# Optimization experiments

Measured on AMD Instinct MI355X. Metric: run time of the kernel, lower is better.

Reference implementation:

```python
import jax, jax.numpy as jnp
import numpy as np

B, S_IMG, S_TXT = 1, 3072, 512
D_MODEL, H, D_HEAD = 3072, 24, 128
INNER = H * D_HEAD
EPS = 1e-5


def rms_norm(x, w):
    # x: [..., D_HEAD]
    var = jnp.mean(jnp.square(x), axis=-1, keepdims=True)
    return x * jax.lax.rsqrt(var + EPS) * w


def apply_rope(x, cos, sin):
    # x: [B,S,H,D]; cos/sin: [S,D]; interleaved (non-neox) rotation
    x1 = x[..., 0::2]
    x2 = x[..., 1::2]
    rot = jnp.stack([-x2, x1], axis=-1).reshape(x.shape)
    c = cos[None, :, None, :]
    s = sin[None, :, None, :]
    return x * c + rot * s


def setup_inputs() -> dict:
    key = jax.random.key(0)
    ks = jax.random.split(key, 12)
    sc = 1.0 / np.sqrt(D_MODEL)
    ang = jax.random.uniform(ks[10], (S_TXT + S_IMG, D_HEAD), jnp.float32, 0.0, 2 * np.pi)
    return {
        "hidden_states": jax.random.normal(ks[0], (B, S_IMG, D_MODEL), jnp.float32),
        "encoder_hidden_states": jax.random.normal(ks[1], (B, S_TXT, D_MODEL), jnp.float32),
        "cos": jnp.cos(ang),
        "sin": jnp.sin(ang),
        "W_qkv": jax.random.normal(ks[2], (3 * INNER, D_MODEL), jnp.float32) * sc,
        "W_add_qkv": jax.random.normal(ks[3], (3 * INNER, D_MODEL), jnp.float32) * sc,
        "b_add_qkv": jnp.zeros((3 * INNER,), jnp.float32),
        "norm_q_w": jnp.ones((D_HEAD,), jnp.float32),
        "norm_k_w": jnp.ones((D_HEAD,), jnp.float32),
        "norm_add_q_w": jnp.ones((D_HEAD,), jnp.float32),
        "norm_add_k_w": jnp.ones((D_HEAD,), jnp.float32),
        "W_out": jax.random.normal(ks[4], (D_MODEL, INNER), jnp.float32) * sc,
        "b_out": jnp.zeros((D_MODEL,), jnp.float32),
        "W_add_out": jax.random.normal(ks[5], (D_MODEL, INNER), jnp.float32) * sc,
        "b_add_out": jnp.zeros((D_MODEL,), jnp.float32),
    }


def reference(hidden_states, encoder_hidden_states, cos, sin,
              W_qkv, W_add_qkv, b_add_qkv,
              norm_q_w, norm_k_w, norm_add_q_w, norm_add_k_w,
              W_out, b_out, W_add_out, b_add_out):
    # fused QKV projections
    qkv = jnp.einsum('bsd,ed->bse', hidden_states, W_qkv)
    q, k, v = jnp.split(qkv, 3, axis=-1)
    eqkv = jnp.einsum('bsd,ed->bse', encoder_hidden_states, W_add_qkv) + b_add_qkv
    eq, ek, ev = jnp.split(eqkv, 3, axis=-1)

    def heads(x):
        return x.reshape(x.shape[0], x.shape[1], H, D_HEAD)

    q, k, v = heads(q), heads(k), heads(v)
    eq, ek, ev = heads(eq), heads(ek), heads(ev)

    # per-head RMSNorm on queries/keys
    q = rms_norm(q, norm_q_w)
    k = rms_norm(k, norm_k_w)
    eq = rms_norm(eq, norm_add_q_w)
    ek = rms_norm(ek, norm_add_k_w)

    # joint concat: text first, then image
    q = jnp.concatenate([eq, q], axis=1)
    k = jnp.concatenate([ek, k], axis=1)
    v = jnp.concatenate([ev, v], axis=1)

    # RoPE on full joint sequence
    q = apply_rope(q, cos, sin)
    k = apply_rope(k, cos, sin)

    # non-causal softmax attention, scale = 1/sqrt(head_dim)
    scale = 1.0 / np.sqrt(D_HEAD)
    scores = jnp.einsum('bqhd,bkhd->bhqk', q, k) * scale
    probs = jax.nn.softmax(scores, axis=-1)
    out = jnp.einsum('bhqk,bkhd->bqhd', probs, v)  # [B,S,H,D]
    out = out.reshape(out.shape[0], out.shape[1], INNER)

    enc_out = out[:, :S_TXT]
    img_out = out[:, S_TXT:]
    enc_out = jnp.einsum('bse,de->bsd', enc_out, W_add_out) + b_add_out
    img_out = jnp.einsum('bse,de->bsd', img_out, W_out) + b_out
    return (img_out, enc_out)
```

## Files before the change

### kernel.cpp

```cpp
#include <hip/hip_runtime.h>


typedef unsigned short u16;
typedef __attribute__((ext_vector_type(2))) unsigned short u16x2;
typedef __attribute__((ext_vector_type(4))) unsigned short u16x4;
typedef __attribute__((ext_vector_type(8))) unsigned short u16x8;
typedef __attribute__((ext_vector_type(8))) short bf16x8;
typedef __attribute__((ext_vector_type(4))) float f32x4;

#define DEV __device__ __forceinline__

DEV u16 f2bf(float f) {
  unsigned u = __builtin_bit_cast(unsigned, f);
  u = (u + 0x7FFFu + ((u >> 16) & 1u)) >> 16;
  return (u16)u;
}
DEV float bf2f(u16 s) { return __builtin_bit_cast(float, (unsigned)s << 16); }

DEV void store_out(u16* p, float v)  { *p = f2bf(v); }
DEV void store_out(float* p, float v) { *p = v; }

#define AS1(p) (const __attribute__((address_space(1))) void*)(p)
#define AS3(p) (__attribute__((address_space(3))) void*)(p)
#define GLL16(g, l) __builtin_amdgcn_global_load_lds(AS1(g), AS3(l), 16, 0, 0)

#define BAR() do { asm volatile("" ::: "memory"); __builtin_amdgcn_s_barrier(); \
                   asm volatile("" ::: "memory"); } while (0)
#define VMC8() asm volatile("s_waitcnt vmcnt(8)" ::: "memory")
#define VMC0() asm volatile("s_waitcnt vmcnt(0)" ::: "memory")

__global__ __launch_bounds__(256) void cvt_kernel(const float* __restrict__ src,
                                                  u16* __restrict__ dst, int n4) {
  int i = blockIdx.x * blockDim.x + threadIdx.x;
  int stride = gridDim.x * blockDim.x;
  for (; i < n4; i += stride) {
    float4 v = reinterpret_cast<const float4*>(src)[i];
    u16x4 o;
    o.x = f2bf(v.x); o.y = f2bf(v.y); o.z = f2bf(v.z); o.w = f2bf(v.w);
    reinterpret_cast<u16x4*>(dst)[i] = o;
  }
}

template <typename OT>
__global__ __launch_bounds__(512, 2) void gemm256(
    const u16* __restrict__ A,
    const u16* __restrict__ Bimg, const u16* __restrict__ Benc,
    const float* __restrict__ biasImg, const float* __restrict__ biasEnc,
    OT* __restrict__ Cimg, OT* __restrict__ Cenc,
    int N, int K, int split, int nwg) {
  const int bid = blockIdx.x;
  const int swz = (bid & 7) * (nwg >> 3) + (bid >> 3);
  const int ntn = N >> 8;
  const int mt = swz / ntn, nt = swz % ntn;
  const int m0 = mt << 8, n0 = nt << 8;
  const u16* B = (m0 < split) ? Benc : Bimg;
  const float* bias = (m0 < split) ? biasEnc : biasImg;

  __shared__ u16 lds[2][2][16384];

  const int tid = threadIdx.x, w = tid >> 6, lane = tid & 63;
  const int wm = w >> 2, wn = w & 3;
  const int q = lane & 15, hi = lane >> 4;
  const size_t ldb = (size_t)K * 2;

  f32x4 acc[8][4];
#pragma unroll
  for (int i = 0; i < 8; ++i)
#pragma unroll
    for (int j = 0; j < 4; ++j)
#pragma unroll
      for (int r = 0; r < 4; ++r) acc[i][j][r] = 0.f;

  auto STAGE = [&](int d, int kt) {
    const char* sA = (const char*)A + (size_t)m0 * ldb + kt * 128;
    const char* sB = (const char*)B + (size_t)n0 * ldb + kt * 128;
    char* dA = (char*)&lds[d][0][0];
    char* dB = (char*)&lds[d][1][0];
#pragma unroll
    for (int j = 0; j < 4; ++j) {
      int base = j * 8192 + w * 1024;
      int off = base + lane * 16;
      int row = off >> 7;
      int src = (off & 127) ^ ((row & 7) << 4);
      GLL16(sA + (size_t)row * ldb + src, dA + base);
      GLL16(sB + (size_t)row * ldb + src, dB + base);
    }
  };
  auto LDA = [&](int d, int i, int ks) -> bf16x8 {
    int row = wm * 128 + i * 16 + q;
    int cb = ks * 64 + hi * 16;
    return *(const bf16x8*)((const char*)&lds[d][0][0] + row * 128 + (cb ^ ((row & 7) << 4)));
  };
  auto LDB = [&](int d, int j, int ks) -> bf16x8 {
    int row = wn * 64 + j * 16 + q;
    int cb = ks * 64 + hi * 16;
    return *(const bf16x8*)((const char*)&lds[d][1][0] + row * 128 + (cb ^ ((row & 7) << 4)));
  };

  auto HALF = [&](int d) {
    bf16x8 bfr[4][2];
#pragma unroll
    for (int ph = 0; ph < 4; ++ph) {
      if (ph == 0) {
#pragma unroll
        for (int j = 0; j < 4; ++j)
#pragma unroll
          for (int ks = 0; ks < 2; ++ks) bfr[j][ks] = LDB(d, j, ks);
      }
      bf16x8 af[2][2];
#pragma unroll
      for (int m = 0; m < 2; ++m)
#pragma unroll
        for (int ks = 0; ks < 2; ++ks) af[m][ks] = LDA(d, 2 * ph + m, ks);
      __builtin_amdgcn_s_setprio(1);
#pragma unroll
      for (int m = 0; m < 2; ++m)
#pragma unroll
        for (int j = 0; j < 4; ++j)
#pragma unroll
          for (int ks = 0; ks < 2; ++ks)
            acc[2 * ph + m][j] = __builtin_amdgcn_mfma_f32_16x16x32_bf16(
                af[m][ks], bfr[j][ks], acc[2 * ph + m][j], 0, 0, 0);
      __builtin_amdgcn_s_setprio(0);
      if (ph < 3) BAR();
    }
  };

  const int NT2 = K >> 7;
  STAGE(0, 0);
  STAGE(1, 1);
  VMC8();
  BAR();
  for (int t = 0; t < NT2; ++t) {
    HALF(0);
    BAR();
    if (t + 1 < NT2) { STAGE(0, 2 * t + 2); VMC8(); }
    else             VMC0();
    BAR();
    HALF(1);
    BAR();
    if (t + 1 < NT2) { STAGE(1, 2 * t + 3); VMC8(); }
    else             VMC0();
    BAR();
  }

#pragma unroll
  for (int i = 0; i < 8; ++i) {
    int rbase = m0 + wm * 128 + i * 16 + (hi << 2);
#pragma unroll
    for (int j = 0; j < 4; ++j) {
      int col = n0 + wn * 64 + j * 16 + q;
      float bv = bias ? bias[col] : 0.f;
#pragma unroll
      for (int r = 0; r < 4; ++r) {
        int row = rbase + r;
        float v = acc[i][j][r] + bv;
        if (row < split) store_out(&Cenc[(size_t)row * N + col], v);
        else             store_out(&Cimg[(size_t)(row - split) * N + col], v);
      }
    }
  }
}

__global__ __launch_bounds__(256) void norm_rope(
    u16* __restrict__ qkv, u16* __restrict__ vt,
    const float* __restrict__ cosT, const float* __restrict__ sinT,
    const float* __restrict__ nqw_img, const float* __restrict__ nkw_img,
    const float* __restrict__ nqw_enc, const float* __restrict__ nkw_enc) {
  const int h = blockIdx.y;
  const int s0 = blockIdx.x * 64;
  const int tid = threadIdx.x, w = tid >> 6, lane = tid & 63;
  const bool enc = (s0 < 512);
  const float* nqw = enc ? nqw_enc : nqw_img;
  const float* nkw = enc ? nkw_enc : nkw_img;
  const float SCL = 0.12751743f;
  const float wq0 = nqw[2 * lane], wq1 = nqw[2 * lane + 1];
  const float wk0 = nkw[2 * lane], wk1 = nkw[2 * lane + 1];
  u16x8 va0, va1, vb0, vb1;
#pragma unroll
  for (int r = 0; r < 16; ++r) {
    const int s = s0 + w * 16 + r;
    const size_t rowb = (size_t)s * 9216 + h * 128 + 2 * lane;
    float2 cv = *(const float2*)&cosT[(size_t)s * 128 + 2 * lane];
    float2 sv = *(const float2*)&sinT[(size_t)s * 128 + 2 * lane];
    {
      u16x2 qu = *(u16x2*)&qkv[rowb];
      float x0 = bf2f(qu.x), x1 = bf2f(qu.y);
      float ss = x0 * x0 + x1 * x1;
#pragma unroll
      for (int d = 1; d < 64; d <<= 1) ss += __shfl_xor(ss, d);
      float rms = rsqrtf(ss * (1.0f / 128.0f) + 1e-5f);
      x0 *= rms * wq0; x1 *= rms * wq1;
      float o0 = (x0 * cv.x - x1 * sv.x) * SCL;
      float o1 = (x1 * cv.y + x0 * sv.y) * SCL;
      u16x2 ou; ou.x = f2bf(o0); ou.y = f2bf(o1);
      *(u16x2*)&qkv[rowb] = ou;
    }
    {
      u16x2 ku = *(u16x2*)&qkv[rowb + 3072];
      float x0 = bf2f(ku.x), x1 = bf2f(ku.y);
      float ss = x0 * x0 + x1 * x1;
#pragma unroll
      for (int d = 1; d < 64; d <<= 1) ss += __shfl_xor(ss, d);
      float rms = rsqrtf(ss * (1.0f / 128.0f) + 1e-5f);
      x0 *= rms * wk0; x1 *= rms * wk1;
      float o0 = x0 * cv.x - x1 * sv.x;
      float o1 = x1 * cv.y + x0 * sv.y;
      u16x2 ou; ou.x = f2bf(o0); ou.y = f2bf(o1);
      *(u16x2*)&qkv[rowb + 3072] = ou;
    }
    {
      u16x2 vu = *(u16x2*)&qkv[rowb + 6144];
      if (r < 8) { va0[r] = vu.x; vb0[r] = vu.y; }
      else       { va1[r - 8] = vu.x; vb1[r - 8] = vu.y; }
    }
  }
  const size_t vbase = (size_t)h * 128 * 3584 + (size_t)(2 * lane) * 3584 + s0 + w * 16;
  *(u16x8*)&vt[vbase]            = va0;
  *(u16x8*)&vt[vbase + 8]        = va1;
  *(u16x8*)&vt[vbase + 3584]     = vb0;
  *(u16x8*)&vt[vbase + 3584 + 8] = vb1;
}

__global__ __launch_bounds__(256, 4) void attn_kernel(
    const u16* __restrict__ qkv, const u16* __restrict__ vt,
    u16* __restrict__ aout) {
  const int bid = blockIdx.x;
  const int qt = bid / 24;
  const int rr = bid % 24;
  const int h = (rr % 8) * 3 + (rr / 8);
  const int tid = threadIdx.x, w = tid >> 6, lane = tid & 63;
  const int qbase = qt * 64 + w * 16;
  const int q = lane & 15, hi = lane >> 4;
  __shared__ u16 Klds[64 * 128];
  __shared__ u16 Vlds[128 * 64];
  __shared__ u16 Plds[4][1024];

  bf16x8 aq[4];
  {
    const u16* qp = qkv + (size_t)(qbase + q) * 9216 + h * 128 + (hi << 3);
#pragma unroll
    for (int ks = 0; ks < 4; ++ks) aq[ks] = *(const bf16x8*)(qp + ks * 32);
  }
  float m_i = -1e30f, l_i = 0.f;
  f32x4 o[8];
#pragma unroll
  for (int dt = 0; dt < 8; ++dt)
#pragma unroll
    for (int r = 0; r < 4; ++r) o[dt][r] = 0.f;
  const size_t vhead = (size_t)h * 128 * 3584;

  for (int kt0 = 0; kt0 < 3584; kt0 += 64) {
    __syncthreads();
#pragma unroll
    for (int j = 0; j < 4; ++j) {
      int base = w * 4096 + j * 1024;
      int off = base + lane * 16;
      int row = off >> 8;
      int src = (off & 255) ^ ((row & 7) << 4);
      GLL16((const char*)(qkv + (size_t)(kt0 + row) * 9216 + 3072 + h * 128) + src, (char*)Klds + base);
    }
#pragma unroll
    for (int j = 0; j < 4; ++j) {
      int base = w * 4096 + j * 1024;
      int off = base + lane * 16;
      int d = off >> 7;
      int src = (off & 127) ^ ((d & 7) << 4);
      GLL16((const char*)(vt + vhead + (size_t)d * 3584 + kt0) + src, (char*)Vlds + base);
    }
    __syncthreads();

    f32x4 sacc[4];
#pragma unroll
    for (int kt = 0; kt < 4; ++kt)
#pragma unroll
      for (int r = 0; r < 4; ++r) sacc[kt][r] = 0.f;
    __builtin_amdgcn_s_setprio(1);
#pragma unroll
    for (int kt = 0; kt < 4; ++kt) {
      const int row = kt * 16 + q;
      bf16x8 bk[4];
#pragma unroll
      for (int ks = 0; ks < 4; ++ks) {
        int cb = (ks * 32 + (hi << 3)) * 2;
        bk[ks] = *(const bf16x8*)((const char*)Klds + (row * 256 + (cb ^ ((row & 7) << 4))));
      }
#pragma unroll
      for (int ks = 0; ks < 4; ++ks)
        sacc[kt] = __builtin_amdgcn_mfma_f32_16x16x32_bf16(bk[ks], aq[ks], sacc[kt], 0, 0, 0);
    }
    __builtin_amdgcn_s_setprio(0);

    float mx = sacc[0][0];
#pragma unroll
    for (int kt = 0; kt < 4; ++kt)
#pragma unroll
      for (int r = 0; r < 4; ++r) mx = fmaxf(mx, sacc[kt][r]);
    mx = fmaxf(mx, __shfl_xor(mx, 16));
    mx = fmaxf(mx, __shfl_xor(mx, 32));
    if (!__all(mx - m_i <= 8.f)) {
      float mnew = fmaxf(m_i, mx);
      float alpha = __builtin_amdgcn_exp2f(m_i - mnew);
      m_i = mnew;
      l_i *= alpha;
#pragma unroll
      for (int r = 0; r < 4; ++r) {
        float ar = __shfl(alpha, (lane & 48) | ((hi << 2) + r));
#pragma unroll
        for (int dt = 0; dt < 8; ++dt) o[dt][r] *= ar;
      }
    }
    float psum = 0.f;
#pragma unroll
    for (int kt = 0; kt < 4; ++kt) {
      u16x4 pw;
#pragma unroll
      for (int r = 0; r < 4; ++r) {
        float p = __builtin_amdgcn_exp2f(sacc[kt][r] - m_i);
        psum += p;
        pw[r] = (u16)(__builtin_bit_cast(unsigned, p) >> 16);
      }
      *(u16x4*)((char*)Plds[w] + ((q * 128 + kt * 32 + hi * 8) ^ ((q & 7) << 4))) = pw;
    }
    psum += __shfl_xor(psum, 16);
    psum += __shfl_xor(psum, 32);
    l_i += psum;

    bf16x8 pa[2];
#pragma unroll
    for (int ks = 0; ks < 2; ++ks) {
      int cb = (ks * 32 + (hi << 3)) * 2;
      pa[ks] = *(const bf16x8*)((const char*)Plds[w] + ((q * 128 + cb) ^ ((q & 7) << 4)));
    }
    __builtin_amdgcn_s_setprio(1);
#pragma unroll
    for (int dt = 0; dt < 8; ++dt) {
      const int vrow = dt * 16 + q;
      bf16x8 bv[2];
#pragma unroll
      for (int ks = 0; ks < 2; ++ks) {
        int cb = (ks * 32 + (hi << 3)) * 2;
        bv[ks] = *(const bf16x8*)((const char*)Vlds + ((vrow * 128 + cb) ^ ((vrow & 7) << 4)));
      }
      o[dt] = __builtin_amdgcn_mfma_f32_16x16x32_bf16(pa[0], bv[0], o[dt], 0, 0, 0);
      o[dt] = __builtin_amdgcn_mfma_f32_16x16x32_bf16(pa[1], bv[1], o[dt], 0, 0, 0);
    }
    __builtin_amdgcn_s_setprio(0);
  }

#pragma unroll
  for (int r = 0; r < 4; ++r) {
    const int q2 = (hi << 2) + r;
    const float lr = __shfl(l_i, (lane & 48) | q2);
    const float inv = 1.0f / lr;
    const int s = qbase + q2;
#pragma unroll
    for (int dt = 0; dt < 8; ++dt) {
      aout[(size_t)s * 3072 + h * 128 + dt * 16 + q] = f2bf(o[dt][r] * inv);
    }
  }
}

extern "C" void kernel_launch(void* const* d_in, const int* in_sizes, int n_in,
                              void* d_out, int out_size, void* d_ws, size_t ws_size,
                              hipStream_t stream) {
  (void)in_sizes; (void)n_in; (void)out_size; (void)ws_size;
  const float* hs    = (const float*)d_in[0];
  const float* ehs   = (const float*)d_in[1];
  const float* cosT  = (const float*)d_in[2];
  const float* sinT  = (const float*)d_in[3];
  const float* Wqkv  = (const float*)d_in[4];
  const float* Wadd  = (const float*)d_in[5];
  const float* bAdd  = (const float*)d_in[6];
  const float* nqw   = (const float*)d_in[7];
  const float* nkw   = (const float*)d_in[8];
  const float* naqw  = (const float*)d_in[9];
  const float* nakw  = (const float*)d_in[10];
  const float* Wout  = (const float*)d_in[11];
  const float* bout  = (const float*)d_in[12];
  const float* Waddo = (const float*)d_in[13];
  const float* baddo = (const float*)d_in[14];

  char* ws = (char*)d_ws;
  u16* Ain = (u16*)(ws);
  u16* WqI = (u16*)(ws + 22020096);
  u16* WqE = WqI + (size_t)9216 * 3072;
  u16* WoI = (u16*)(ws + 135266304);
  u16* WoE = WoI + (size_t)3072 * 3072;
  u16* qkv = (u16*)(ws + 173015040);
  u16* vt   = Ain;
  u16* aout = WqI;

  cvt_kernel<<<1024, 256, 0, stream>>>(ehs,   Ain,                      512 * 3072 / 4);
  cvt_kernel<<<1024, 256, 0, stream>>>(hs,    Ain + (size_t)512 * 3072, 3072 * 3072 / 4);
  cvt_kernel<<<2048, 256, 0, stream>>>(Wqkv,  WqI, 9216 * 3072 / 4);
  cvt_kernel<<<2048, 256, 0, stream>>>(Wadd,  WqE, 9216 * 3072 / 4);
  cvt_kernel<<<1024, 256, 0, stream>>>(Wout,  WoI, 3072 * 3072 / 4);
  cvt_kernel<<<1024, 256, 0, stream>>>(Waddo, WoE, 3072 * 3072 / 4);

  gemm256<u16><<<dim3(504), 512, 0, stream>>>(Ain, WqI, WqE, nullptr, bAdd,
                                              qkv + (size_t)512 * 9216, qkv, 9216, 3072, 512, 504);
  norm_rope<<<dim3(56, 24), 256, 0, stream>>>(qkv, vt, cosT, sinT, nqw, nkw, naqw, nakw);
  attn_kernel<<<dim3(1344), 256, 0, stream>>>(qkv, vt, aout);
  float* outp = (float*)d_out;
  gemm256<float><<<dim3(168), 512, 0, stream>>>(aout, WoI, WoE, bout, baddo,
                                                outp, outp + (size_t)3072 * 3072, 3072, 3072, 512, 168);
}
```

Measured before the change: 738.4 us.

## Pipeline K/V tile loads against compute in attention and use MFMA-native LDS layout

Restructures the attention inner loop so the next K tile is prefetched while softmax and PV run, and the next V tile while the next QK runs. Separate barriers and vmcnt waits replace the single load-then-sync step per tile. K, V and P are also stored in LDS in a fragment-ordered layout that removes the XOR swizzle address math. This adds extra barriers per iteration, and the unswizzled layout may introduce LDS bank conflicts on the global_load_lds writes or the reads.

Result: slower. 757.4 us (+2.6%).

```diff
diff --git a/kernel.cpp b/kernel.cpp
--- a/kernel.cpp
+++ b/kernel.cpp
@@ -27,6 +27,7 @@
 #define BAR() do { asm volatile("" ::: "memory"); __builtin_amdgcn_s_barrier(); \
                    asm volatile("" ::: "memory"); } while (0)
 #define VMC8() asm volatile("s_waitcnt vmcnt(8)" ::: "memory")
+#define VMC4() asm volatile("s_waitcnt vmcnt(4)" ::: "memory")
 #define VMC0() asm volatile("s_waitcnt vmcnt(0)" ::: "memory")
 
 __global__ __launch_bounds__(256) void cvt_kernel(const float* __restrict__ src,
@@ -232,8 +233,8 @@
   const int tid = threadIdx.x, w = tid >> 6, lane = tid & 63;
   const int qbase = qt * 64 + w * 16;
   const int q = lane & 15, hi = lane >> 4;
-  __shared__ u16 Klds[64 * 128];
-  __shared__ u16 Vlds[128 * 64];
+  __shared__ u16 Klds[8192];
+  __shared__ u16 Vlds[8192];
   __shared__ u16 Plds[4][1024];
 
   bf16x8 aq[4];
@@ -250,26 +251,26 @@
     for (int r = 0; r < 4; ++r) o[dt][r] = 0.f;
   const size_t vhead = (size_t)h * 128 * 3584;
 
-  for (int kt0 = 0; kt0 < 3584; kt0 += 64) {
-    __syncthreads();
-#pragma unroll
-    for (int j = 0; j < 4; ++j) {
-      int base = w * 4096 + j * 1024;
-      int off = base + lane * 16;
-      int row = off >> 8;
-      int src = (off & 255) ^ ((row & 7) << 4);
-      GLL16((const char*)(qkv + (size_t)(kt0 + row) * 9216 + 3072 + h * 128) + src, (char*)Klds + base);
-    }
-#pragma unroll
-    for (int j = 0; j < 4; ++j) {
-      int base = w * 4096 + j * 1024;
-      int off = base + lane * 16;
-      int d = off >> 7;
-      int src = (off & 127) ^ ((d & 7) << 4);
-      GLL16((const char*)(vt + vhead + (size_t)d * 3584 + kt0) + src, (char*)Vlds + base);
-    }
-    __syncthreads();
-
+  auto STAGE_K = [&](int kt0) {
+    const char* src = (const char*)(qkv + (size_t)(kt0 + w * 16 + q) * 9216 + 3072 + h * 128) + (hi << 4);
+    char* dst = (char*)Klds + w * 4096 + lane * 16;
+#pragma unroll
+    for (int j = 0; j < 4; ++j) GLL16(src + j * 64, dst + j * 1024);
+  };
+  auto STAGE_V = [&](int kt0) {
+    const char* vsrc = (const char*)(vt + vhead + kt0) + (hi << 4);
+    char* dst = (char*)Vlds + w * 4096 + lane * 16;
+#pragma unroll
+    for (int j = 0; j < 4; ++j)
+      GLL16(vsrc + (size_t)((w * 2 + (j >> 1)) * 16 + q) * 7168 + (j & 1) * 64, dst + j * 1024);
+  };
+
+  const int NT = 56;
+  STAGE_K(0);
+  STAGE_V(0);
+  VMC4();
+  BAR();
+  for (int t = 0; t < NT; ++t) {
     f32x4 sacc[4];
 #pragma unroll
     for (int kt = 0; kt < 4; ++kt)
@@ -278,18 +279,19 @@
     __builtin_amdgcn_s_setprio(1);
 #pragma unroll
     for (int kt = 0; kt < 4; ++kt) {
-      const int row = kt * 16 + q;
       bf16x8 bk[4];
 #pragma unroll
-      for (int ks = 0; ks < 4; ++ks) {
-        int cb = (ks * 32 + (hi << 3)) * 2;
-        bk[ks] = *(const bf16x8*)((const char*)Klds + (row * 256 + (cb ^ ((row & 7) << 4))));
-      }
+      for (int ks = 0; ks < 4; ++ks)
+        bk[ks] = *(const bf16x8*)((const char*)Klds + kt * 4096 + ks * 1024 + hi * 256 + q * 16);
 #pragma unroll
       for (int ks = 0; ks < 4; ++ks)
         sacc[kt] = __builtin_amdgcn_mfma_f32_16x16x32_bf16(bk[ks], aq[ks], sacc[kt], 0, 0, 0);
     }
     __builtin_amdgcn_s_setprio(0);
+    BAR();
+    if (t + 1 < NT) { STAGE_K((t + 1) * 64); VMC4(); }
+    else            VMC0();
+    BAR();
 
     float mx = sacc[0][0];
 #pragma unroll
@@ -320,7 +322,8 @@
         psum += p;
         pw[r] = (u16)(__builtin_bit_cast(unsigned, p) >> 16);
       }
-      *(u16x4*)((char*)Plds[w] + ((q * 128 + kt * 32 + hi * 8) ^ ((q & 7) << 4))) = pw;
+      const int c = kt * 2 + (hi >> 1);
+      *(u16x4*)((char*)Plds[w] + ((c >> 2) * 1024 + (c & 3) * 256 + q * 16 + (hi & 1) * 8)) = pw;
     }
     psum += __shfl_xor(psum, 16);
     psum += __shfl_xor(psum, 32);
@@ -328,24 +331,23 @@
 
     bf16x8 pa[2];
 #pragma unroll
-    for (int ks = 0; ks < 2; ++ks) {
-      int cb = (ks * 32 + (hi << 3)) * 2;
-      pa[ks] = *(const bf16x8*)((const char*)Plds[w] + ((q * 128 + cb) ^ ((q & 7) << 4)));
-    }
+    for (int ks = 0; ks < 2; ++ks)
+      pa[ks] = *(const bf16x8*)((const char*)Plds[w] + ks * 1024 + hi * 256 + q * 16);
     __builtin_amdgcn_s_setprio(1);
 #pragma unroll
     for (int dt = 0; dt < 8; ++dt) {
-      const int vrow = dt * 16 + q;
       bf16x8 bv[2];
 #pragma unroll
-      for (int ks = 0; ks < 2; ++ks) {
-        int cb = (ks * 32 + (hi << 3)) * 2;
-        bv[ks] = *(const bf16x8*)((const char*)Vlds + ((vrow * 128 + cb) ^ ((vrow & 7) << 4)));
-      }
+      for (int ks = 0; ks < 2; ++ks)
+        bv[ks] = *(const bf16x8*)((const char*)Vlds + dt * 2048 + ks * 1024 + hi * 256 + q * 16);
       o[dt] = __builtin_amdgcn_mfma_f32_16x16x32_bf16(pa[0], bv[0], o[dt], 0, 0, 0);
       o[dt] = __builtin_amdgcn_mfma_f32_16x16x32_bf16(pa[1], bv[1], o[dt], 0, 0, 0);
     }
     __builtin_amdgcn_s_setprio(0);
+    BAR();
+    if (t + 1 < NT) { STAGE_V((t + 1) * 64); VMC4(); }
+    else            VMC0();
+    BAR();
   }
 
 #pragma unroll
```
